# Performance work log

Hardware: AMD Instinct MI355X
Metric: run time of the kernel (lower is better)

The kernel has to match this reference:

```python
import jax, jax.numpy as jnp
import numpy as np

N_BLOCKS = 96
N = N_BLOCKS ** 2          # number of image blocks = n_blocks^2
D = 1024                   # feature dim (fixed by Linear(1024+1, 128))
EPS_COS = 1e-6             # eps of F.cosine_similarity
EPS_BN = 1e-5              # BatchNorm1d eps


def setup_inputs() -> dict:
    key = jax.random.key(0)
    ks = jax.random.split(key, 6)
    return {
        "features": jax.random.normal(ks[0], (N, D), dtype=jnp.float32),
        "scores": jax.random.uniform(ks[1], (N,), dtype=jnp.float32),
        "W1": jax.random.normal(ks[2], (D + 1, 128), dtype=jnp.float32) * 0.03,
        "b1": jnp.zeros((128,), jnp.float32),
        "g1": jnp.ones((128,), jnp.float32),
        "be1": jnp.zeros((128,), jnp.float32),
        "W2": jax.random.normal(ks[3], (128, 64), dtype=jnp.float32) * 0.08,
        "b2": jnp.zeros((64,), jnp.float32),
        "g2": jnp.ones((64,), jnp.float32),
        "be2": jnp.zeros((64,), jnp.float32),
        "W3": jax.random.normal(ks[4], (64, 1), dtype=jnp.float32) * 0.12,
        "b3": jnp.zeros((1,), jnp.float32),
    }


def _gaussian_similarity(features):
    # Vectorized form of the O(N^2) pairwise loop:
    #   cos_ij = <f_i, f_j> / max(|f_i||f_j|, eps)
    #   sigma^2 = D * (0.5 + 0.5 * cos)  ->  2*sigma^2 = D * (1 + cos)
    #   sim_ij = exp(-|f_i - f_j|^2 / (2*sigma^2)),  sim_ii = 1
    sq = jnp.sum(features * features, axis=-1)          # [N] squared norms
    gram = features @ features.T                          # [N, N] big GEMM
    norms = jnp.sqrt(sq)
    cos = gram / jnp.maximum(norms[:, None] * norms[None, :], EPS_COS)
    d2 = jnp.maximum(sq[:, None] + sq[None, :] - 2.0 * gram, 0.0)
    denom = jnp.maximum(jnp.float32(D) * (1.0 + cos), EPS_COS)
    sim = jnp.exp(-d2 / denom)
    eye = jnp.eye(sim.shape[0], dtype=bool)
    return jnp.where(eye, jnp.float32(1.0), sim)


def _bn_eval(h, gamma, beta):
    # BatchNorm1d in eval mode with init running stats (mean=0, var=1).
    return gamma * (h / jnp.sqrt(1.0 + EPS_BN)) + beta


def reference(features, scores, W1, b1, g1, be1, W2, b2, g2, be2, W3, b3):
    sim = _gaussian_similarity(features)                  # [N, N]
    x = jnp.concatenate([features, scores[:, None]], axis=1)  # [N, D+1]
    h = jax.nn.relu(_bn_eval(x @ W1 + b1, g1, be1))       # [N, 128]
    h = jax.nn.relu(_bn_eval(h @ W2 + b2, g2, be2))       # [N, 64]
    agg = jax.nn.sigmoid(h @ W3 + b3)[:, 0]               # [N]
    sim_mean = jnp.mean(sim, axis=1)                      # [N]
    # Torch broadcast [N,1] * [N] -> [N,N], then .mean() == mean(agg)*mean(sim_mean)
    return jnp.mean(agg) * jnp.mean(sim_mean)


if __name__ == "__main__":
    out = reference(**setup_inputs())
    print(out)
```

## Files before the change

kernel.cpp:

```cpp
#include <hip/hip_runtime.h>

#define N_IMG 9216
#define DFEAT 1024
#define NBR2 72
#define NPAIR4 2628

typedef __attribute__((ext_vector_type(8))) short short8;
typedef __attribute__((ext_vector_type(4))) float floatx4;
typedef __attribute__((ext_vector_type(16))) float floatx16;
typedef __attribute__((ext_vector_type(4))) int intx4;
typedef __attribute__((ext_vector_type(8))) int intx8;

#define C1F 0.0014088818759657845f
#define C2F 0.05308355472172724f

__device__ __forceinline__ void async_copy16(const void* g, void* l) {
  __builtin_amdgcn_global_load_lds((const __attribute__((address_space(1))) void*)g,
                                   (__attribute__((address_space(3))) void*)l,
                                   16, 0, 0);
}

__device__ __forceinline__ unsigned short f2bf(float x) {
  union { float f; unsigned u; } a; a.f = x;
  unsigned u = a.u;
  u += 0x7fffu + ((u >> 16) & 1u);
  return (unsigned short)(u >> 16);
}

__device__ __forceinline__ unsigned q4(float z) {
  unsigned sg = (__float_as_uint(z) >> 28) & 8u;
  float a = fabsf(z);
  unsigned c = (a < 0.25f) ? 0u : (a < 0.75f) ? 1u : (a < 1.25f) ? 2u :
               (a < 1.75f) ? 3u : (a < 2.5f)  ? 4u : (a < 3.5f)  ? 5u :
               (a < 5.0f)  ? 6u : 7u;
  return c | sg;
}
__device__ __forceinline__ unsigned short pk4(float4 v, float sc) {
  unsigned b0 = q4(v.x * sc) | (q4(v.y * sc) << 4);
  unsigned b1 = q4(v.z * sc) | (q4(v.w * sc) << 4);
  return (unsigned short)(b0 | (b1 << 8));
}

__global__ __launch_bounds__(256) void convert_prep(const float* __restrict__ f,
                                                    const float* __restrict__ W1,
                                                    unsigned char* __restrict__ fbT,
                                                    float* __restrict__ sL,
                                                    float* __restrict__ pL,
                                                    unsigned short* __restrict__ W1t,
                                                    double* __restrict__ sums,
                                                    unsigned* __restrict__ ctr) {
  int b = blockIdx.x, t = threadIdx.x;
  if (b < 2304) {
    int lane = t & 63, wave = t >> 6;
    int row = b * 4 + wave;
    const float4* src = (const float4*)f + (size_t)row * 256;
    float4 v0 = src[lane], v1 = src[64 + lane], v2 = src[128 + lane], v3 = src[192 + lane];
    float s = v0.x * v0.x + v0.y * v0.y + v0.z * v0.z + v0.w * v0.w
            + v1.x * v1.x + v1.y * v1.y + v1.z * v1.z + v1.w * v1.w
            + v2.x * v2.x + v2.y * v2.y + v2.z * v2.z + v2.w * v2.w
            + v3.x * v3.x + v3.y * v3.y + v3.z * v3.z + v3.w * v3.w;
#pragma unroll
    for (int off = 32; off > 0; off >>= 1) s += __shfl_xor(s, off, 64);
    float zsc = rsqrtf(s) * 32.f;
    unsigned short u0 = pk4(v0, zsc), u1 = pk4(v1, zsc),
                   u2 = pk4(v2, zsc), u3 = pk4(v3, zsc);
    unsigned char* tb = fbT + (size_t)(row >> 5) * 16384 + (row & 31) * 32 + (lane & 15) * 2;
    int ko = (lane >> 4) * 1024;
    *(unsigned short*)(tb + ko) = u0;
    *(unsigned short*)(tb + ko + 4096) = u1;
    *(unsigned short*)(tb + ko + 8192) = u2;
    *(unsigned short*)(tb + ko + 12288) = u3;
    if (lane == 0) {
      sL[row] = s * C1F;
      pL[row] = sqrtf(s) * C2F;
    }
  } else {
    int j = b - 2304;
    if (j == 0) {
      if (t < 2) sums[t] = 0.0;
      if (t == 2) *ctr = 0u;
    }
    for (int k = t; k < DFEAT; k += 256)
      W1t[(size_t)j * DFEAT + k] = f2bf(W1[(size_t)k * 128 + j]);
  }
}

__global__ __launch_bounds__(256, 3) void gram_sim(const unsigned char* __restrict__ fbT,
                                                   const float* __restrict__ sL,
                                                   const float* __restrict__ pL,
                                                   double* __restrict__ sums) {
  __shared__ float sA[128], pA[128], sB[128], pB[128];
  __shared__ float wpart[4];

  int bid = blockIdx.x, t = threadIdx.x, lane = t & 63, wave = t >> 6;
  int xcd = bid & 7, ii = bid >> 3;
  int L = (xcd < 4 ? xcd * 329 : 1316 + (xcd - 4) * 328) + ii;
  int bcol = (int)((sqrtf(8.f * (float)L + 1.f) - 1.f) * 0.5f);
  while ((bcol + 1) * (bcol + 2) / 2 <= L) bcol++;
  while (bcol * (bcol + 1) / 2 > L) bcol--;
  int brow = L - bcol * (bcol + 1) / 2;

  if (t < 128) { sA[t] = sL[brow * 128 + t]; pA[t] = pL[brow * 128 + t]; }
  else { int u = t - 128; sB[u] = sL[bcol * 128 + u]; pB[u] = pL[bcol * 128 + u]; }
  __syncthreads();

  const int r32 = lane & 31, kh = lane >> 5;
  const int loff = r32 * 32 + kh * 16;
  const int wr = (wave & 1) * 64, wc = (wave >> 1) * 64;

  const unsigned char* pa0 = fbT + (size_t)(brow * 4 + (wr >> 5)) * 16384 + loff;
  const unsigned char* pa1 = pa0 + 16384;
  const unsigned char* pb0 = fbT + (size_t)(bcol * 4 + (wc >> 5)) * 16384 + loff;
  const unsigned char* pb1 = pb0 + 16384;

  floatx16 acc[2][2];
#pragma unroll
  for (int mi = 0; mi < 2; mi++)
#pragma unroll
    for (int ni = 0; ni < 2; ni++)
#pragma unroll
      for (int e = 0; e < 16; e++) acc[mi][ni][e] = 0.f;

  union u8x { intx8 v8; intx4 q[2]; };
  u8x A8[2], B8[2];
#pragma unroll
  for (int mi = 0; mi < 2; mi++) A8[mi].q[1] = (intx4){0, 0, 0, 0};
#pragma unroll
  for (int ni = 0; ni < 2; ni++) B8[ni].q[1] = (intx4){0, 0, 0, 0};

  intx4 bA[3][2], bB[3][2];
#define LDSET(s, kb)                                                          \
  {                                                                           \
    const int o = (kb) * 1024;                                                \
    bA[s][0] = *(const intx4*)(pa0 + o); bA[s][1] = *(const intx4*)(pa1 + o); \
    bB[s][0] = *(const intx4*)(pb0 + o); bB[s][1] = *(const intx4*)(pb1 + o); \
  }
  LDSET(0, 0)
  LDSET(1, 1)
#pragma unroll
  for (int kb = 0; kb < 16; kb++) {
    const int cur = kb % 3, nxt = (kb + 2) % 3;
    if (kb < 14) LDSET(nxt, kb + 2)
    A8[0].q[0] = bA[cur][0]; A8[1].q[0] = bA[cur][1];
    B8[0].q[0] = bB[cur][0]; B8[1].q[0] = bB[cur][1];
#pragma unroll
    for (int mi = 0; mi < 2; mi++)
#pragma unroll
      for (int ni = 0; ni < 2; ni++)
        acc[mi][ni] = __builtin_amdgcn_mfma_scale_f32_32x32x64_f8f6f4(
            A8[mi].v8, B8[ni].v8, acc[mi][ni], 4, 4,
            0, 0x7F7F7F7F, 0, 0x7F7F7F7F);
  }
#undef LDSET

  const bool diag = (brow == bcol);
  float lsum = 0.f;
#pragma unroll
  for (int ni = 0; ni < 2; ni++) {
    int j_loc = wc + ni * 32 + r32;
    float sj = sB[j_loc], pj = pB[j_loc];
#pragma unroll
    for (int mi = 0; mi < 2; mi++) {
      int rbase = wr + mi * 32 + 4 * kh;
#pragma unroll
      for (int reg = 0; reg < 16; reg++) {
        int i_loc = rbase + (reg & 3) + 8 * (reg >> 2);
        float g = acc[mi][ni][reg];
        float si = sA[i_loc], pi = pA[i_loc];
        float r = __builtin_amdgcn_rcpf(1024.f + g);
        float del = pi * pj;
        float gam = si + sj + del;
        float sim = __builtin_amdgcn_exp2f(fmaf(-1024.f, gam * r, del));
        if (!diag) {
          lsum += sim;
        } else {
          lsum += (i_loc < j_loc) ? 2.f * sim : (i_loc == j_loc ? 1.f : 0.f);
        }
      }
    }
  }
  if (!diag) lsum *= 2.f;
#pragma unroll
  for (int off = 32; off > 0; off >>= 1) lsum += __shfl_down(lsum, off, 64);
  if (lane == 0) wpart[wave] = lsum;
  __syncthreads();
  if (t == 0)
    atomicAdd(&sums[0], (double)(wpart[0] + wpart[1] + wpart[2] + wpart[3]));
}

__global__ __launch_bounds__(256) void mlp_full(const float* __restrict__ f,
                                                const unsigned short* __restrict__ W1t,
                                                const float* __restrict__ scores,
                                                const float* __restrict__ W1,
                                                const float* __restrict__ b1,
                                                const float* __restrict__ g1,
                                                const float* __restrict__ be1,
                                                const float* __restrict__ W2, const float* __restrict__ b2,
                                                const float* __restrict__ g2, const float* __restrict__ be2,
                                                const float* __restrict__ W3, const float* __restrict__ b3,
                                                double* __restrict__ sums,
                                                unsigned* __restrict__ ctr,
                                                float* __restrict__ out) {
  int r0 = blockIdx.x * 32;

  __shared__ __align__(16) float As32[2 * 32 * 64];
  __shared__ __align__(16) unsigned short Bs[2 * 128 * 64];
  __shared__ float h1s[32][128];
  __shared__ float h2s[32][65];
  __shared__ float sc[32], b1s[128], g1s[128], be1s[128], wls[128], ls[32];

  int t = threadIdx.x, lane = t & 63, wave = t >> 6;
  if (t < 32) sc[t] = scores[r0 + t];
  if (t < 128) {
    b1s[t] = b1[t]; g1s[t] = g1[t]; be1s[t] = be1[t];
    wls[t] = W1[(size_t)DFEAT * 128 + t];
  }
  __syncthreads();

  floatx4 acc[4];
#pragma unroll
  for (int b = 0; b < 4; b++) acc[b] = (floatx4){0.f, 0.f, 0.f, 0.f};

  const int wr = (wave & 1) * 16, wc = (wave >> 1) * 64;

#define MSTAGE(buf, kk)                                                     \
  {                                                                         \
    const int k0_ = (kk) * 64;                                              \
    int c = t, rA = c >> 4, p = c & 15, l = p ^ (rA & 15);                  \
    async_copy16(f + (size_t)(r0 + rA) * DFEAT + k0_ + l * 4,               \
                 (char*)As32 + (buf) * 8192 + c * 16);                      \
    c = t + 256; rA = c >> 4; p = c & 15; l = p ^ (rA & 15);                \
    async_copy16(f + (size_t)(r0 + rA) * DFEAT + k0_ + l * 4,               \
                 (char*)As32 + (buf) * 8192 + c * 16);                      \
    _Pragma("unroll")                                                       \
    for (int q2 = 0; q2 < 4; q2++) {                                        \
      int cc = t + q2 * 256, rB = cc >> 3, pp = cc & 7, ll = pp ^ (rB & 7); \
      async_copy16(W1t + (size_t)rB * DFEAT + k0_ + ll * 8,                 \
                   (char*)Bs + (buf) * 16384 + cc * 16);                    \
    }                                                                       \
  }

  MSTAGE(0, 0)
  MSTAGE(1, 1)
  for (int kk = 0; kk < 16; kk++) {
    if (kk < 15) asm volatile("s_waitcnt vmcnt(6)" ::: "memory");
    else         asm volatile("s_waitcnt vmcnt(0)" ::: "memory");
    __builtin_amdgcn_s_barrier();
    __builtin_amdgcn_sched_barrier(0);
    const int bufF = (kk & 1) * 2048;
    const int bufS = (kk & 1) * 8192;

    const int mrow = lane & 15;
#pragma unroll
    for (int ks = 0; ks < 2; ks++) {
      const int kq = ks * 32 + (lane >> 4) * 8;
      short8 a, b[4];
      {
        int row = wr + mrow;
        int l0 = kq >> 2;
        int p0 = l0 ^ (row & 15), p1 = (l0 + 1) ^ (row & 15);
        float4 f0 = *(const float4*)&As32[bufF + row * 64 + p0 * 4];
        float4 f1 = *(const float4*)&As32[bufF + row * 64 + p1 * 4];
        a[0] = (short)f2bf(f0.x); a[1] = (short)f2bf(f0.y);
        a[2] = (short)f2bf(f0.z); a[3] = (short)f2bf(f0.w);
        a[4] = (short)f2bf(f1.x); a[5] = (short)f2bf(f1.y);
        a[6] = (short)f2bf(f1.z); a[7] = (short)f2bf(f1.w);
      }
#pragma unroll
      for (int nt = 0; nt < 4; nt++) {
        int row = wc + nt * 16 + mrow;
        int p = (kq >> 3) ^ (row & 7);
        b[nt] = *(const short8*)&Bs[bufS + row * 64 + p * 8];
      }
#pragma unroll
      for (int nt = 0; nt < 4; nt++)
        acc[nt] = __builtin_amdgcn_mfma_f32_16x16x32_bf16(a, b[nt], acc[nt], 0, 0, 0);
    }
    __builtin_amdgcn_sched_barrier(0);
    __builtin_amdgcn_s_barrier();
    __builtin_amdgcn_sched_barrier(0);
    if (kk < 14) MSTAGE((kk & 1), kk + 2)
  }
#undef MSTAGE

  const float inv = 1.0f / sqrtf(1.0f + 1e-5f);
  const int rq = (lane >> 4) * 4, cn = lane & 15;
#pragma unroll
  for (int nt = 0; nt < 4; nt++) {
    int j = wc + nt * 16 + cn;
    float bj = b1s[j], gj = g1s[j] * inv, bej = be1s[j], wj = wls[j];
#pragma unroll
    for (int rr = 0; rr < 4; rr++) {
      int iL = wr + rq + rr;
      float pre = acc[nt][rr] + sc[iL] * wj + bj;
      h1s[iL][j] = fmaxf(gj * pre + bej, 0.f);
    }
  }
  __syncthreads();

  {
    int j = t & 63, rg = (t >> 6) * 8;
    float a2[8];
#pragma unroll
    for (int rr = 0; rr < 8; rr++) a2[rr] = 0.f;
    for (int k = 0; k < 128; k++) {
      float w = W2[k * 64 + j];
#pragma unroll
      for (int rr = 0; rr < 8; rr++) a2[rr] = fmaf(h1s[rg + rr][k], w, a2[rr]);
    }
    float scv = g2[j] * inv, bi = b2[j], be = be2[j];
#pragma unroll
    for (int rr = 0; rr < 8; rr++)
      h2s[rg + rr][j] = fmaxf(scv * (a2[rr] + bi) + be, 0.f);
  }
  __syncthreads();

  if (t < 32) {
    float z = b3[0];
#pragma unroll
    for (int k = 0; k < 64; k++) z = fmaf(h2s[t][k], W3[k], z);
    ls[t] = 1.f / (1.f + __expf(-z));
  }
  __syncthreads();
  if (t == 0) {
    float s = 0.f;
#pragma unroll
    for (int iL = 0; iL < 32; iL++) s += ls[iL];
    atomicAdd(&sums[1], (double)s);
    __threadfence();
    unsigned prev = atomicAdd(ctr, 1u);
    if (prev == 287u) {
      __threadfence();
      double s0 = ((volatile double*)sums)[0];
      double s1 = ((volatile double*)sums)[1];
      out[0] = (float)((s1 / (double)N_IMG) * (s0 / ((double)N_IMG * (double)N_IMG)));
    }
  }
}

extern "C" void kernel_launch(void* const* d_in, const int* in_sizes, int n_in,
                              void* d_out, int out_size, void* d_ws, size_t ws_size,
                              hipStream_t stream) {
  const float* f      = (const float*)d_in[0];
  const float* scores = (const float*)d_in[1];
  const float* W1 = (const float*)d_in[2];
  const float* b1 = (const float*)d_in[3];
  const float* g1 = (const float*)d_in[4];
  const float* be1 = (const float*)d_in[5];
  const float* W2 = (const float*)d_in[6];
  const float* b2 = (const float*)d_in[7];
  const float* g2 = (const float*)d_in[8];
  const float* be2 = (const float*)d_in[9];
  const float* W3 = (const float*)d_in[10];
  const float* b3 = (const float*)d_in[11];

  char* ws = (char*)d_ws;
  unsigned char* fbT  = (unsigned char*)ws;
  float* sL           = (float*)(ws + 4718592);
  float* pL           = (float*)(ws + 4755456);
  unsigned short* W1t = (unsigned short*)(ws + 4792320);
  double* sums        = (double*)(ws + 5054464);
  unsigned* ctr       = (unsigned*)(ws + 5054480);

  convert_prep<<<2432, 256, 0, stream>>>(f, W1, fbT, sL, pL, W1t, sums, ctr);
  gram_sim<<<NPAIR4, 256, 0, stream>>>(fbT, sL, pL, sums);
  mlp_full<<<288, 256, 0, stream>>>(f, W1t, scores, W1, b1, g1, be1,
                                    W2, b2, g2, be2, W3, b3, sums, ctr,
                                    (float*)d_out);
}
```

Baseline: 189.5 us.

## Enlarge gram_sim block tile from 128x128 to 256x256 with 4x4 MFMA per wave

```diff
diff --git a/kernel.cpp b/kernel.cpp
--- a/kernel.cpp
+++ b/kernel.cpp
@@ -2,8 +2,8 @@
 
 #define N_IMG 9216
 #define DFEAT 1024
-#define NBR2 72
-#define NPAIR4 2628
+#define NBP 36
+#define NPAIR2 666
 
 typedef __attribute__((ext_vector_type(8))) short short8;
 typedef __attribute__((ext_vector_type(4))) float floatx4;
@@ -85,55 +85,61 @@
   }
 }
 
-__global__ __launch_bounds__(256, 3) void gram_sim(const unsigned char* __restrict__ fbT,
-                                                   const float* __restrict__ sL,
-                                                   const float* __restrict__ pL,
-                                                   double* __restrict__ sums) {
-  __shared__ float sA[128], pA[128], sB[128], pB[128];
+__global__ __launch_bounds__(256) void gram_sim(const unsigned char* __restrict__ fbT,
+                                                const float* __restrict__ sL,
+                                                const float* __restrict__ pL,
+                                                double* __restrict__ sums) {
+  __shared__ float sA[256], pA[256], sB[256], pB[256];
   __shared__ float wpart[4];
 
   int bid = blockIdx.x, t = threadIdx.x, lane = t & 63, wave = t >> 6;
   int xcd = bid & 7, ii = bid >> 3;
-  int L = (xcd < 4 ? xcd * 329 : 1316 + (xcd - 4) * 328) + ii;
-  int bcol = (int)((sqrtf(8.f * (float)L + 1.f) - 1.f) * 0.5f);
-  while ((bcol + 1) * (bcol + 2) / 2 <= L) bcol++;
-  while (bcol * (bcol + 1) / 2 > L) bcol--;
-  int brow = L - bcol * (bcol + 1) / 2;
-
-  if (t < 128) { sA[t] = sL[brow * 128 + t]; pA[t] = pL[brow * 128 + t]; }
-  else { int u = t - 128; sB[u] = sL[bcol * 128 + u]; pB[u] = pL[bcol * 128 + u]; }
+  int L = (xcd < 2 ? xcd * 84 : 168 + (xcd - 2) * 83) + ii;
+  int rem = L, bcol = 0;
+  while (rem > bcol) { rem -= (bcol + 1); bcol++; }
+  int brow = rem;
+
+  sA[t] = sL[brow * 256 + t]; pA[t] = pL[brow * 256 + t];
+  sB[t] = sL[bcol * 256 + t]; pB[t] = pL[bcol * 256 + t];
   __syncthreads();
 
   const int r32 = lane & 31, kh = lane >> 5;
   const int loff = r32 * 32 + kh * 16;
-  const int wr = (wave & 1) * 64, wc = (wave >> 1) * 64;
-
-  const unsigned char* pa0 = fbT + (size_t)(brow * 4 + (wr >> 5)) * 16384 + loff;
-  const unsigned char* pa1 = pa0 + 16384;
-  const unsigned char* pb0 = fbT + (size_t)(bcol * 4 + (wc >> 5)) * 16384 + loff;
-  const unsigned char* pb1 = pb0 + 16384;
-
-  floatx16 acc[2][2];
-#pragma unroll
-  for (int mi = 0; mi < 2; mi++)
-#pragma unroll
-    for (int ni = 0; ni < 2; ni++)
+  const int wr = (wave & 1) * 128, wc = (wave >> 1) * 128;
+
+  const unsigned char* pa[4];
+  const unsigned char* pb[4];
+#pragma unroll
+  for (int mi = 0; mi < 4; mi++)
+    pa[mi] = fbT + (size_t)(brow * 8 + (wave & 1) * 4 + mi) * 16384 + loff;
+#pragma unroll
+  for (int ni = 0; ni < 4; ni++)
+    pb[ni] = fbT + (size_t)(bcol * 8 + (wave >> 1) * 4 + ni) * 16384 + loff;
+
+  floatx16 acc[4][4];
+#pragma unroll
+  for (int mi = 0; mi < 4; mi++)
+#pragma unroll
+    for (int ni = 0; ni < 4; ni++)
 #pragma unroll
       for (int e = 0; e < 16; e++) acc[mi][ni][e] = 0.f;
 
   union u8x { intx8 v8; intx4 q[2]; };
-  u8x A8[2], B8[2];
-#pragma unroll
-  for (int mi = 0; mi < 2; mi++) A8[mi].q[1] = (intx4){0, 0, 0, 0};
-#pragma unroll
-  for (int ni = 0; ni < 2; ni++) B8[ni].q[1] = (intx4){0, 0, 0, 0};
-
-  intx4 bA[3][2], bB[3][2];
+  u8x A8[4], B8[4];
+#pragma unroll
+  for (int i = 0; i < 4; i++) {
+    A8[i].q[1] = (intx4){0, 0, 0, 0};
+    B8[i].q[1] = (intx4){0, 0, 0, 0};
+  }
+
+  intx4 bA[3][4], bB[3][4];
 #define LDSET(s, kb)                                                          \
   {                                                                           \
     const int o = (kb) * 1024;                                                \
-    bA[s][0] = *(const intx4*)(pa0 + o); bA[s][1] = *(const intx4*)(pa1 + o); \
-    bB[s][0] = *(const intx4*)(pb0 + o); bB[s][1] = *(const intx4*)(pb1 + o); \
+    bA[s][0] = *(const intx4*)(pa[0] + o); bA[s][1] = *(const intx4*)(pa[1] + o); \
+    bA[s][2] = *(const intx4*)(pa[2] + o); bA[s][3] = *(const intx4*)(pa[3] + o); \
+    bB[s][0] = *(const intx4*)(pb[0] + o); bB[s][1] = *(const intx4*)(pb[1] + o); \
+    bB[s][2] = *(const intx4*)(pb[2] + o); bB[s][3] = *(const intx4*)(pb[3] + o); \
   }
   LDSET(0, 0)
   LDSET(1, 1)
@@ -141,12 +147,15 @@
   for (int kb = 0; kb < 16; kb++) {
     const int cur = kb % 3, nxt = (kb + 2) % 3;
     if (kb < 14) LDSET(nxt, kb + 2)
-    A8[0].q[0] = bA[cur][0]; A8[1].q[0] = bA[cur][1];
-    B8[0].q[0] = bB[cur][0]; B8[1].q[0] = bB[cur][1];
-#pragma unroll
-    for (int mi = 0; mi < 2; mi++)
-#pragma unroll
-      for (int ni = 0; ni < 2; ni++)
+#pragma unroll
+    for (int i = 0; i < 4; i++) {
+      A8[i].q[0] = bA[cur][i];
+      B8[i].q[0] = bB[cur][i];
+    }
+#pragma unroll
+    for (int mi = 0; mi < 4; mi++)
+#pragma unroll
+      for (int ni = 0; ni < 4; ni++)
         acc[mi][ni] = __builtin_amdgcn_mfma_scale_f32_32x32x64_f8f6f4(
             A8[mi].v8, B8[ni].v8, acc[mi][ni], 4, 4,
             0, 0x7F7F7F7F, 0, 0x7F7F7F7F);
@@ -156,11 +165,11 @@
   const bool diag = (brow == bcol);
   float lsum = 0.f;
 #pragma unroll
-  for (int ni = 0; ni < 2; ni++) {
+  for (int ni = 0; ni < 4; ni++) {
     int j_loc = wc + ni * 32 + r32;
     float sj = sB[j_loc], pj = pB[j_loc];
 #pragma unroll
-    for (int mi = 0; mi < 2; mi++) {
+    for (int mi = 0; mi < 4; mi++) {
       int rbase = wr + mi * 32 + 4 * kh;
 #pragma unroll
       for (int reg = 0; reg < 16; reg++) {
@@ -363,7 +372,7 @@
   unsigned* ctr       = (unsigned*)(ws + 5054480);
 
   convert_prep<<<2432, 256, 0, stream>>>(f, W1, fbT, sL, pL, W1t, sums, ctr);
-  gram_sim<<<NPAIR4, 256, 0, stream>>>(fbT, sL, pL, sums);
+  gram_sim<<<NPAIR2, 256, 0, stream>>>(fbT, sL, pL, sums);
   mlp_full<<<288, 256, 0, stream>>>(f, W1t, scores, W1, b1, g1, be1,
                                     W2, b2, g2, be2, W3, b3, sums, ctr,
                                     (float*)d_out);
```

New measurement: 189.9 us. No clear change (+0.2%).
